# Kernel optimization log

Hardware: AMD Instinct MI355X
Metric: run time of the kernel (lower is better)

Reference implementation:

```python
import jax, jax.numpy as jnp
import numpy as np

B, IN, H, L = 4096, 1024, 1024, 8


def setup_inputs() -> dict:
    key = jax.random.key(0)
    k1, k2, k3, k4, k5 = jax.random.split(key, 5)
    scale = 0.02
    inputs = jax.random.normal(k1, (B, IN), dtype=jnp.float32)
    # Stacked gate weights, order [f, i, o, g] along first axis (torch Linear: y = x @ W.T + b)
    W = jax.random.normal(k2, (4 * H, IN), dtype=jnp.float32) * scale   # input->gates
    bW = jax.random.normal(k3, (4 * H,), dtype=jnp.float32) * scale
    U = jax.random.normal(k4, (4 * H, H), dtype=jnp.float32) * scale    # hidden->gates
    bU = jax.random.normal(k5, (4 * H,), dtype=jnp.float32) * scale
    return {"inputs": inputs, "W": W, "bW": bW, "U": U, "bU": bU, "num_layers": L}


def reference(inputs, W, bW, U, bU, num_layers):
    batch = inputs.shape[0]
    hid = U.shape[1]
    # Input projection is loop-invariant: compute once. [B, 4H]
    x_proj = jnp.einsum('bi,gi->bg', inputs, W) + bW
    xf, xi, xo, xg = jnp.split(x_proj, 4, axis=1)

    def step(carry, _):
        ht, ct = carry
        h_proj = jnp.einsum('bh,gh->bg', ht, U) + bU  # [B, 4H]
        hf, hi, ho, hg = jnp.split(h_proj, 4, axis=1)
        f = jax.nn.sigmoid(xf + hf)
        i = jax.nn.sigmoid(xi + hi)
        o = jax.nn.sigmoid(xo + ho)
        g = jnp.tanh(xg + hg)
        ct_new = f * ct + i * g
        ht_new = o * jnp.tanh(ct_new)
        return (ht_new, ct_new), None

    h0 = jnp.zeros((batch, hid), dtype=inputs.dtype)
    c0 = jnp.zeros((batch, hid), dtype=inputs.dtype)
    (ht, ct), _ = jax.lax.scan(step, (h0, c0), None, length=num_layers)
    return ht, ct
```

## Files before the change

### kernel.cpp

```cpp
#include <hip/hip_runtime.h>
#include <hip/hip_bf16.h>

typedef __bf16 bf16x8 __attribute__((ext_vector_type(8)));
typedef float f32x4 __attribute__((ext_vector_type(4)));

#define DEVI static __device__ __forceinline__

DEVI void load_lds16(const void* g, void* l) {
  __builtin_amdgcn_global_load_lds(
      (const __attribute__((address_space(1))) void*)g,
      (__attribute__((address_space(3))) void*)l, 16, 0, 0);
}

DEVI unsigned short f2b(float f) { return __bfloat16_as_ushort(__float2bfloat16(f)); }
DEVI float b2f(unsigned short u) {
  union { unsigned int i; float f; } c;
  c.i = ((unsigned int)u) << 16;
  return c.f;
}
DEVI float sigm(float x) { return 1.0f / (1.0f + __expf(-x)); }
DEVI float tanh_fast(float x) { return 2.0f / (1.0f + __expf(-2.0f * x)) - 1.0f; }

DEVI int swz(int L) { return L ^ (((L >> 7) & 7) << 4); }

__global__ __launch_bounds__(256) void cast_kernel(const float* __restrict__ src,
                                                   unsigned short* __restrict__ dst,
                                                   int n4) {
  const int i = blockIdx.x * 256 + threadIdx.x;
  if (i >= n4) return;
  const float4 v = reinterpret_cast<const float4*>(src)[i];
  ushort4 o;
  o.x = f2b(v.x); o.y = f2b(v.y); o.z = f2b(v.z); o.w = f2b(v.w);
  reinterpret_cast<ushort4*>(dst)[i] = o;
}

__global__ __launch_bounds__(256) void cast_perm_kernel(const float* __restrict__ src,
                                                        unsigned short* __restrict__ dst) {
  const int i = blockIdx.x * 256 + threadIdx.x;
  const int r = i >> 8;
  const int cw = i & 255;
  const float4 v = reinterpret_cast<const float4*>(src)[i];
  const int rp = ((r & 1023) << 2) + (r >> 10);
  ushort4 o;
  o.x = f2b(v.x); o.y = f2b(v.y); o.z = f2b(v.z); o.w = f2b(v.w);
  *reinterpret_cast<ushort4*>(&dst[(size_t)rp * 1024 + (cw << 2)]) = o;
}

__global__ __launch_bounds__(256) void bias_prep(const float* __restrict__ bW,
                                                 const float* __restrict__ bU,
                                                 float* __restrict__ bp) {
  const int i = blockIdx.x * 256 + threadIdx.x;
  const int h = i >> 2, g = i & 3;
  bp[i] = bW[g * 1024 + h] + bU[g * 1024 + h];
}

template <bool FUSED, bool LAST>
__global__ __launch_bounds__(512, 2) void gemm256(
    const unsigned short* __restrict__ A,
    const unsigned short* __restrict__ Bm,
    unsigned short* __restrict__ Cout,
    const unsigned short* __restrict__ xproj,
    const float* __restrict__ bp,
    float* __restrict__ ct,
    unsigned short* __restrict__ htout,
    float* __restrict__ out) {
  constexpr int K = 1024, N = 4096;
  constexpr int NPH = K / 32;
  __shared__ unsigned char lds[256 * 528];

  const int tid = threadIdx.x;
  const int lane = tid & 63;
  const int wave = tid >> 6;
  const int wr = wave >> 2;
  const int wc = wave & 3;

  const int bid = blockIdx.x;
  const int sw = (bid & 7) * 32 + (bid >> 3);
  const int brow = (sw >> 4) * 256;
  const int bcol = (sw & 15) * 256;

  const int physA0 = tid * 16;
  const int physA1 = 8192 + tid * 16;
  const int physB0 = 16384 + tid * 16;
  const int physB1 = 24576 + tid * 16;
  const int LA0 = swz(physA0), LA1 = swz(physA1);
  const int LB0 = swz(physB0 - 16384), LB1 = swz(physB1 - 16384);
  const unsigned char* pA0 = (const unsigned char*)A + (size_t)(brow + (LA0 >> 6)) * (K * 2) + (LA0 & 63);
  const unsigned char* pA1 = (const unsigned char*)A + (size_t)(brow + (LA1 >> 6)) * (K * 2) + (LA1 & 63);
  const unsigned char* pB0 = (const unsigned char*)Bm + (size_t)(bcol + (LB0 >> 6)) * (K * 2) + (LB0 & 63);
  const unsigned char* pB1 = (const unsigned char*)Bm + (size_t)(bcol + (LB1 >> 6)) * (K * 2) + (LB1 & 63);

  const int s16 = (lane >> 4) * 16;
  int offA[8], offB[4];
#pragma unroll
  for (int m = 0; m < 8; ++m) {
    const int row = wr * 128 + m * 16 + (lane & 15);
    offA[m] = swz(row * 64 + s16);
  }
#pragma unroll
  for (int n = 0; n < 4; ++n) {
    const int row = wc * 64 + n * 16 + (lane & 15);
    offB[n] = 16384 + swz(row * 64 + s16);
  }

  f32x4 acc[8][4] = {};

  auto STAGE = [&](int q) {
    unsigned char* sb = lds + (q & 3) * 32768;
    const size_t kb = (size_t)q * 64;
    load_lds16(pA0 + kb, sb + physA0);
    load_lds16(pA1 + kb, sb + physA1);
    load_lds16(pB0 + kb, sb + physB0);
    load_lds16(pB1 + kb, sb + physB1);
  };

  STAGE(0); STAGE(1); STAGE(2);
  asm volatile("s_waitcnt vmcnt(8)" ::: "memory");
  __builtin_amdgcn_s_barrier();
  __builtin_amdgcn_sched_barrier(0);

  for (int p = 0; p < NPH; ++p) {
    if (p + 3 < NPH) STAGE(p + 3);

    const unsigned char* sl = lds + (p & 3) * 32768;
    bf16x8 af[8], bf[4];
#pragma unroll
    for (int n = 0; n < 4; ++n) bf[n] = *reinterpret_cast<const bf16x8*>(sl + offB[n]);
#pragma unroll
    for (int m = 0; m < 8; ++m) af[m] = *reinterpret_cast<const bf16x8*>(sl + offA[m]);

    __builtin_amdgcn_s_setprio(1);
#pragma unroll
    for (int m = 0; m < 8; ++m)
#pragma unroll
      for (int n = 0; n < 4; ++n)
        acc[m][n] = __builtin_amdgcn_mfma_f32_16x16x32_bf16(af[m], bf[n], acc[m][n], 0, 0, 0);
    __builtin_amdgcn_s_setprio(0);

    if (p < NPH - 1) {
      if (p < NPH - 3)
        asm volatile("s_waitcnt vmcnt(8)" ::: "memory");
      else if (p == NPH - 3)
        asm volatile("s_waitcnt vmcnt(4)" ::: "memory");
      else
        asm volatile("s_waitcnt vmcnt(0)" ::: "memory");
      __builtin_amdgcn_s_barrier();
      __builtin_amdgcn_sched_barrier(0);
    }
  }

  __syncthreads();
  unsigned short* cs = (unsigned short*)lds;
  {
    const int c0 = wc * 64 + (lane & 15);
    const int r00 = wr * 128 + ((lane >> 4) << 2);
#pragma unroll
    for (int m = 0; m < 8; ++m)
#pragma unroll
      for (int n = 0; n < 4; ++n) {
        const int rr = r00 + m * 16;
        const int cc = c0 + n * 16;
#pragma unroll
        for (int r = 0; r < 4; ++r) cs[(rr + r) * 264 + cc] = f2b(acc[m][n][r]);
      }
  }
  __syncthreads();

  if constexpr (!FUSED) {
#pragma unroll
    for (int j = 0; j < 16; ++j) {
      const int g = tid + (j << 9);
      const int row = g >> 5, gc = g & 31;
      const uint4 v = *reinterpret_cast<const uint4*>(&cs[row * 264 + gc * 8]);
      *reinterpret_cast<uint4*>(&Cout[(size_t)(brow + row) * N + bcol + gc * 8]) = v;
    }
  } else {
    const int hbase = bcol >> 2;
    for (int j = 0; j < 32; ++j) {
      const int q = tid + (j << 9);
      const int row = q >> 6;
      const int hh = q & 63;
      const ushort4 pv = *reinterpret_cast<const ushort4*>(&cs[row * 264 + hh * 4]);
      const ushort4 xv = *reinterpret_cast<const ushort4*>(&xproj[(size_t)(brow + row) * N + bcol + hh * 4]);
      const float4 bpv = *reinterpret_cast<const float4*>(&bp[bcol + hh * 4]);
      const int ci = (brow + row) * 1024 + hbase + hh;
      const float c_old = ct[ci];
      const float sf = b2f(pv.x) + b2f(xv.x) + bpv.x;
      const float si = b2f(pv.y) + b2f(xv.y) + bpv.y;
      const float so = b2f(pv.z) + b2f(xv.z) + bpv.z;
      const float sg = b2f(pv.w) + b2f(xv.w) + bpv.w;
      const float f = sigm(sf);
      const float ii = sigm(si);
      const float o = sigm(so);
      const float gg = tanh_fast(sg);
      const float c = fmaf(f, c_old, ii * gg);
      const float h = o * tanh_fast(c);
      ct[ci] = c;
      if constexpr (LAST) {
        out[ci] = h;
        out[4194304 + ci] = c;
      } else {
        htout[ci] = f2b(h);
      }
    }
  }
}

__global__ __launch_bounds__(256) void gates_first(
    const unsigned short* __restrict__ xproj, const float* __restrict__ bp,
    float* __restrict__ ct, unsigned short* __restrict__ ht) {
  const int i = blockIdx.x * 256 + threadIdx.x;
  const int b = i >> 8;
  const int h0 = (i & 255) << 2;
  const size_t xbase = (size_t)b * 4096 + ((size_t)h0 << 2);
  float cn[4], hn[4];
#pragma unroll
  for (int k = 0; k < 4; ++k) {
    const ushort4 pv = *reinterpret_cast<const ushort4*>(&xproj[xbase + k * 4]);
    const float4 bpv = *reinterpret_cast<const float4*>(&bp[(h0 + k) * 4]);
    const float f = sigm(b2f(pv.x) + bpv.x);  (void)f;
    const float ii = sigm(b2f(pv.y) + bpv.y);
    const float o = sigm(b2f(pv.z) + bpv.z);
    const float gg = tanh_fast(b2f(pv.w) + bpv.w);
    const float c = ii * gg;
    cn[k] = c;
    hn[k] = o * tanh_fast(c);
  }
  const int ci = b * 1024 + h0;
  *reinterpret_cast<float4*>(&ct[ci]) = make_float4(cn[0], cn[1], cn[2], cn[3]);
  ushort4 hb;
  hb.x = f2b(hn[0]); hb.y = f2b(hn[1]); hb.z = f2b(hn[2]); hb.w = f2b(hn[3]);
  *reinterpret_cast<ushort4*>(&ht[ci]) = hb;
}

extern "C" void kernel_launch(void* const* d_in, const int* in_sizes, int n_in,
                              void* d_out, int out_size, void* d_ws, size_t ws_size,
                              hipStream_t stream) {
  const float* x = (const float*)d_in[0];
  const float* W = (const float*)d_in[1];
  const float* bW = (const float*)d_in[2];
  const float* U = (const float*)d_in[3];
  const float* bU = (const float*)d_in[4];
  float* out = (float*)d_out;

  char* w = (char*)d_ws;
  const size_t MB = 1ull << 20;
  unsigned short* xb = (unsigned short*)(w + 0 * MB);
  unsigned short* Wbp = (unsigned short*)(w + 8 * MB);
  unsigned short* Ubp = (unsigned short*)(w + 16 * MB);
  unsigned short* xproj = (unsigned short*)(w + 24 * MB);
  float* ct = (float*)(w + 56 * MB);
  unsigned short* htA = (unsigned short*)(w + 72 * MB);
  unsigned short* htB = (unsigned short*)(w + 80 * MB);
  float* bp = (float*)(w + 88 * MB);

  const int n4 = (4096 * 1024) / 4;
  cast_kernel<<<4096, 256, 0, stream>>>(x, xb, n4);
  cast_perm_kernel<<<4096, 256, 0, stream>>>(W, Wbp);
  cast_perm_kernel<<<4096, 256, 0, stream>>>(U, Ubp);
  bias_prep<<<16, 256, 0, stream>>>(bW, bU, bp);

  gemm256<false, false><<<256, 512, 0, stream>>>(xb, Wbp, xproj, nullptr, nullptr, nullptr, nullptr, nullptr);
  gates_first<<<4096, 256, 0, stream>>>(xproj, bp, ct, htA);

  const unsigned short* hin = htA;
  unsigned short* hout = htB;
  for (int t = 1; t <= 6; ++t) {
    gemm256<true, false><<<256, 512, 0, stream>>>(hin, Ubp, nullptr, xproj, bp, ct, hout, nullptr);
    const unsigned short* tmp = hout;
    hout = (unsigned short*)hin;
    hin = tmp;
  }
  gemm256<true, true><<<256, 512, 0, stream>>>(hin, Ubp, nullptr, xproj, bp, ct, nullptr, out);
}
```

Measured before the change: 428.8 us.

## Shrink GEMM tile to 128x256 with 4 waves and triple buffering

Changes the GEMM block tile from 256x256 with 8 waves to 128x256 with 4 waves, launching 512 blocks instead of 256. The LDS pipeline drops from 4 slots with prefetch depth 3 to 3 slots with depth 2, cutting LDS per block so more blocks can be resident per CU. The aim is better occupancy and load balance across the 256 CUs, at the cost of reloading the B (weight) tile twice as often per output and a shallower prefetch that may expose memory latency. It also drops an unused sigmoid in gates_first and partially unrolls the fused epilogue loop.

After: 443.1 us. 3.3% more time.

```diff
diff --git a/kernel.cpp b/kernel.cpp
--- a/kernel.cpp
+++ b/kernel.cpp
@@ -55,7 +55,7 @@
 }
 
 template <bool FUSED, bool LAST>
-__global__ __launch_bounds__(512, 2) void gemm256(
+__global__ __launch_bounds__(256, 2) void gemm256(
     const unsigned short* __restrict__ A,
     const unsigned short* __restrict__ Bm,
     unsigned short* __restrict__ Cout,
@@ -66,63 +66,59 @@
     float* __restrict__ out) {
   constexpr int K = 1024, N = 4096;
   constexpr int NPH = K / 32;
-  __shared__ unsigned char lds[256 * 528];
+  constexpr int SLOT = 24576;
+  __shared__ unsigned char lds[3 * SLOT];
 
   const int tid = threadIdx.x;
   const int lane = tid & 63;
-  const int wave = tid >> 6;
-  const int wr = wave >> 2;
-  const int wc = wave & 3;
+  const int wc = tid >> 6;
 
   const int bid = blockIdx.x;
-  const int sw = (bid & 7) * 32 + (bid >> 3);
-  const int brow = (sw >> 4) * 256;
+  const int sw = (bid & 7) * 64 + (bid >> 3);
+  const int brow = (sw >> 4) * 128;
   const int bcol = (sw & 15) * 256;
 
   const int physA0 = tid * 16;
-  const int physA1 = 8192 + tid * 16;
-  const int physB0 = 16384 + tid * 16;
-  const int physB1 = 24576 + tid * 16;
+  const int physA1 = 4096 + tid * 16;
   const int LA0 = swz(physA0), LA1 = swz(physA1);
-  const int LB0 = swz(physB0 - 16384), LB1 = swz(physB1 - 16384);
   const unsigned char* pA0 = (const unsigned char*)A + (size_t)(brow + (LA0 >> 6)) * (K * 2) + (LA0 & 63);
   const unsigned char* pA1 = (const unsigned char*)A + (size_t)(brow + (LA1 >> 6)) * (K * 2) + (LA1 & 63);
-  const unsigned char* pB0 = (const unsigned char*)Bm + (size_t)(bcol + (LB0 >> 6)) * (K * 2) + (LB0 & 63);
-  const unsigned char* pB1 = (const unsigned char*)Bm + (size_t)(bcol + (LB1 >> 6)) * (K * 2) + (LB1 & 63);
+  int physB[4];
+  const unsigned char* pB[4];
+#pragma unroll
+  for (int q = 0; q < 4; ++q) {
+    physB[q] = 8192 + q * 4096 + tid * 16;
+    const int LB = swz(physB[q] - 8192);
+    pB[q] = (const unsigned char*)Bm + (size_t)(bcol + (LB >> 6)) * (K * 2) + (LB & 63);
+  }
 
   const int s16 = (lane >> 4) * 16;
   int offA[8], offB[4];
 #pragma unroll
-  for (int m = 0; m < 8; ++m) {
-    const int row = wr * 128 + m * 16 + (lane & 15);
-    offA[m] = swz(row * 64 + s16);
-  }
-#pragma unroll
-  for (int n = 0; n < 4; ++n) {
-    const int row = wc * 64 + n * 16 + (lane & 15);
-    offB[n] = 16384 + swz(row * 64 + s16);
-  }
+  for (int m = 0; m < 8; ++m) offA[m] = swz((m * 16 + (lane & 15)) * 64 + s16);
+#pragma unroll
+  for (int n = 0; n < 4; ++n) offB[n] = 8192 + swz(((wc * 64) + n * 16 + (lane & 15)) * 64 + s16);
 
   f32x4 acc[8][4] = {};
 
   auto STAGE = [&](int q) {
-    unsigned char* sb = lds + (q & 3) * 32768;
+    unsigned char* sb = lds + (q % 3) * SLOT;
     const size_t kb = (size_t)q * 64;
     load_lds16(pA0 + kb, sb + physA0);
     load_lds16(pA1 + kb, sb + physA1);
-    load_lds16(pB0 + kb, sb + physB0);
-    load_lds16(pB1 + kb, sb + physB1);
+#pragma unroll
+    for (int j = 0; j < 4; ++j) load_lds16(pB[j] + kb, sb + physB[j]);
   };
 
-  STAGE(0); STAGE(1); STAGE(2);
-  asm volatile("s_waitcnt vmcnt(8)" ::: "memory");
+  STAGE(0); STAGE(1);
+  asm volatile("s_waitcnt vmcnt(6)" ::: "memory");
   __builtin_amdgcn_s_barrier();
   __builtin_amdgcn_sched_barrier(0);
 
   for (int p = 0; p < NPH; ++p) {
-    if (p + 3 < NPH) STAGE(p + 3);
-
-    const unsigned char* sl = lds + (p & 3) * 32768;
+    if (p + 2 < NPH) STAGE(p + 2);
+
+    const unsigned char* sl = lds + (p % 3) * SLOT;
     bf16x8 af[8], bf[4];
 #pragma unroll
     for (int n = 0; n < 4; ++n) bf[n] = *reinterpret_cast<const bf16x8*>(sl + offB[n]);
@@ -138,10 +134,8 @@
     __builtin_amdgcn_s_setprio(0);
 
     if (p < NPH - 1) {
-      if (p < NPH - 3)
-        asm volatile("s_waitcnt vmcnt(8)" ::: "memory");
-      else if (p == NPH - 3)
-        asm volatile("s_waitcnt vmcnt(4)" ::: "memory");
+      if (p <= NPH - 3)
+        asm volatile("s_waitcnt vmcnt(6)" ::: "memory");
       else
         asm volatile("s_waitcnt vmcnt(0)" ::: "memory");
       __builtin_amdgcn_s_barrier();
@@ -153,12 +147,12 @@
   unsigned short* cs = (unsigned short*)lds;
   {
     const int c0 = wc * 64 + (lane & 15);
-    const int r00 = wr * 128 + ((lane >> 4) << 2);
+    const int crow0 = (lane >> 4) * 4;
 #pragma unroll
     for (int m = 0; m < 8; ++m)
 #pragma unroll
       for (int n = 0; n < 4; ++n) {
-        const int rr = r00 + m * 16;
+        const int rr = m * 16 + crow0;
         const int cc = c0 + n * 16;
 #pragma unroll
         for (int r = 0; r < 4; ++r) cs[(rr + r) * 264 + cc] = f2b(acc[m][n][r]);
@@ -169,15 +163,16 @@
   if constexpr (!FUSED) {
 #pragma unroll
     for (int j = 0; j < 16; ++j) {
-      const int g = tid + (j << 9);
+      const int g = tid + (j << 8);
       const int row = g >> 5, gc = g & 31;
       const uint4 v = *reinterpret_cast<const uint4*>(&cs[row * 264 + gc * 8]);
       *reinterpret_cast<uint4*>(&Cout[(size_t)(brow + row) * N + bcol + gc * 8]) = v;
     }
   } else {
     const int hbase = bcol >> 2;
+#pragma unroll 4
     for (int j = 0; j < 32; ++j) {
-      const int q = tid + (j << 9);
+      const int q = tid + (j << 8);
       const int row = q >> 6;
       const int hh = q & 63;
       const ushort4 pv = *reinterpret_cast<const ushort4*>(&cs[row * 264 + hh * 4]);
@@ -218,7 +213,6 @@
   for (int k = 0; k < 4; ++k) {
     const ushort4 pv = *reinterpret_cast<const ushort4*>(&xproj[xbase + k * 4]);
     const float4 bpv = *reinterpret_cast<const float4*>(&bp[(h0 + k) * 4]);
-    const float f = sigm(b2f(pv.x) + bpv.x);  (void)f;
     const float ii = sigm(b2f(pv.y) + bpv.y);
     const float o = sigm(b2f(pv.z) + bpv.z);
     const float gg = tanh_fast(b2f(pv.w) + bpv.w);
@@ -260,16 +254,16 @@
   cast_perm_kernel<<<4096, 256, 0, stream>>>(U, Ubp);
   bias_prep<<<16, 256, 0, stream>>>(bW, bU, bp);
 
-  gemm256<false, false><<<256, 512, 0, stream>>>(xb, Wbp, xproj, nullptr, nullptr, nullptr, nullptr, nullptr);
+  gemm256<false, false><<<512, 256, 0, stream>>>(xb, Wbp, xproj, nullptr, nullptr, nullptr, nullptr, nullptr);
   gates_first<<<4096, 256, 0, stream>>>(xproj, bp, ct, htA);
 
   const unsigned short* hin = htA;
   unsigned short* hout = htB;
   for (int t = 1; t <= 6; ++t) {
-    gemm256<true, false><<<256, 512, 0, stream>>>(hin, Ubp, nullptr, xproj, bp, ct, hout, nullptr);
+    gemm256<true, false><<<512, 256, 0, stream>>>(hin, Ubp, nullptr, xproj, bp, ct, hout, nullptr);
     const unsigned short* tmp = hout;
     hout = (unsigned short*)hin;
     hin = tmp;
   }
-  gemm256<true, true><<<256, 512, 0, stream>>>(hin, Ubp, nullptr, xproj, bp, ct, nullptr, out);
-}
+  gemm256<true, true><<<512, 256, 0, stream>>>(hin, Ubp, nullptr, xproj, bp, ct, nullptr, out);
+}
```

## Fuse first-step gates into input GEMM, fold bias into xproj, store cell state in bf16

Applied to the files above, without the earlier changes.

The input-projection GEMM now also computes the first LSTM step's gates and writes h and c directly, which removes the separate gates_first kernel and one full re-read of xproj. The combined bias is added once and stored into the bf16 xproj buffer, so later steps no longer load the bias. The cell state is kept in bf16 instead of fp32, which halves its read/write traffic per step. Storing c in bf16 across steps loses precision and can accumulate error over the recurrence.

Result: faster. 402.6 us (-6.1%).

```diff
diff --git a/kernel.cpp b/kernel.cpp
--- a/kernel.cpp
+++ b/kernel.cpp
@@ -54,14 +54,14 @@
   bp[i] = bW[g * 1024 + h] + bU[g * 1024 + h];
 }
 
-template <bool FUSED, bool LAST>
+template <int MODE>
 __global__ __launch_bounds__(512, 2) void gemm256(
     const unsigned short* __restrict__ A,
     const unsigned short* __restrict__ Bm,
-    unsigned short* __restrict__ Cout,
-    const unsigned short* __restrict__ xproj,
+    const unsigned short* __restrict__ xpb_r,
+    unsigned short* __restrict__ xpb_w,
     const float* __restrict__ bp,
-    float* __restrict__ ct,
+    unsigned short* __restrict__ ct,
     unsigned short* __restrict__ htout,
     float* __restrict__ out) {
   constexpr int K = 1024, N = 4096;
@@ -166,71 +166,46 @@
   }
   __syncthreads();
 
-  if constexpr (!FUSED) {
-#pragma unroll
-    for (int j = 0; j < 16; ++j) {
-      const int g = tid + (j << 9);
-      const int row = g >> 5, gc = g & 31;
-      const uint4 v = *reinterpret_cast<const uint4*>(&cs[row * 264 + gc * 8]);
-      *reinterpret_cast<uint4*>(&Cout[(size_t)(brow + row) * N + bcol + gc * 8]) = v;
+  const int hbase = bcol >> 2;
+#pragma unroll 4
+  for (int j = 0; j < 32; ++j) {
+    const int q = tid + (j << 9);
+    const int row = q >> 6;
+    const int hh = q & 63;
+    const ushort4 pv = *reinterpret_cast<const ushort4*>(&cs[row * 264 + hh * 4]);
+    const int ci = (brow + row) * 1024 + hbase + hh;
+    float sf, si, so, sg;
+    if constexpr (MODE == 0) {
+      const float4 bpv = *reinterpret_cast<const float4*>(&bp[bcol + hh * 4]);
+      sf = b2f(pv.x) + bpv.x;
+      si = b2f(pv.y) + bpv.y;
+      so = b2f(pv.z) + bpv.z;
+      sg = b2f(pv.w) + bpv.w;
+      ushort4 xo;
+      xo.x = f2b(sf); xo.y = f2b(si); xo.z = f2b(so); xo.w = f2b(sg);
+      *reinterpret_cast<ushort4*>(&xpb_w[(size_t)(brow + row) * N + bcol + hh * 4]) = xo;
+    } else {
+      const ushort4 xv = *reinterpret_cast<const ushort4*>(&xpb_r[(size_t)(brow + row) * N + bcol + hh * 4]);
+      sf = b2f(pv.x) + b2f(xv.x);
+      si = b2f(pv.y) + b2f(xv.y);
+      so = b2f(pv.z) + b2f(xv.z);
+      sg = b2f(pv.w) + b2f(xv.w);
     }
-  } else {
-    const int hbase = bcol >> 2;
-    for (int j = 0; j < 32; ++j) {
-      const int q = tid + (j << 9);
-      const int row = q >> 6;
-      const int hh = q & 63;
-      const ushort4 pv = *reinterpret_cast<const ushort4*>(&cs[row * 264 + hh * 4]);
-      const ushort4 xv = *reinterpret_cast<const ushort4*>(&xproj[(size_t)(brow + row) * N + bcol + hh * 4]);
-      const float4 bpv = *reinterpret_cast<const float4*>(&bp[bcol + hh * 4]);
-      const int ci = (brow + row) * 1024 + hbase + hh;
-      const float c_old = ct[ci];
-      const float sf = b2f(pv.x) + b2f(xv.x) + bpv.x;
-      const float si = b2f(pv.y) + b2f(xv.y) + bpv.y;
-      const float so = b2f(pv.z) + b2f(xv.z) + bpv.z;
-      const float sg = b2f(pv.w) + b2f(xv.w) + bpv.w;
-      const float f = sigm(sf);
-      const float ii = sigm(si);
-      const float o = sigm(so);
-      const float gg = tanh_fast(sg);
-      const float c = fmaf(f, c_old, ii * gg);
-      const float h = o * tanh_fast(c);
-      ct[ci] = c;
-      if constexpr (LAST) {
-        out[ci] = h;
-        out[4194304 + ci] = c;
-      } else {
-        htout[ci] = f2b(h);
-      }
+    const float c_old = (MODE == 0) ? 0.0f : b2f(ct[ci]);
+    const float f = sigm(sf);
+    const float ii = sigm(si);
+    const float o = sigm(so);
+    const float gg = tanh_fast(sg);
+    const float c = fmaf(f, c_old, ii * gg);
+    const float h = o * tanh_fast(c);
+    if constexpr (MODE == 2) {
+      out[ci] = h;
+      out[4194304 + ci] = c;
+    } else {
+      ct[ci] = f2b(c);
+      htout[ci] = f2b(h);
     }
   }
-}
-
-__global__ __launch_bounds__(256) void gates_first(
-    const unsigned short* __restrict__ xproj, const float* __restrict__ bp,
-    float* __restrict__ ct, unsigned short* __restrict__ ht) {
-  const int i = blockIdx.x * 256 + threadIdx.x;
-  const int b = i >> 8;
-  const int h0 = (i & 255) << 2;
-  const size_t xbase = (size_t)b * 4096 + ((size_t)h0 << 2);
-  float cn[4], hn[4];
-#pragma unroll
-  for (int k = 0; k < 4; ++k) {
-    const ushort4 pv = *reinterpret_cast<const ushort4*>(&xproj[xbase + k * 4]);
-    const float4 bpv = *reinterpret_cast<const float4*>(&bp[(h0 + k) * 4]);
-    const float f = sigm(b2f(pv.x) + bpv.x);  (void)f;
-    const float ii = sigm(b2f(pv.y) + bpv.y);
-    const float o = sigm(b2f(pv.z) + bpv.z);
-    const float gg = tanh_fast(b2f(pv.w) + bpv.w);
-    const float c = ii * gg;
-    cn[k] = c;
-    hn[k] = o * tanh_fast(c);
-  }
-  const int ci = b * 1024 + h0;
-  *reinterpret_cast<float4*>(&ct[ci]) = make_float4(cn[0], cn[1], cn[2], cn[3]);
-  ushort4 hb;
-  hb.x = f2b(hn[0]); hb.y = f2b(hn[1]); hb.z = f2b(hn[2]); hb.w = f2b(hn[3]);
-  *reinterpret_cast<ushort4*>(&ht[ci]) = hb;
 }
 
 extern "C" void kernel_launch(void* const* d_in, const int* in_sizes, int n_in,
@@ -248,11 +223,11 @@
   unsigned short* xb = (unsigned short*)(w + 0 * MB);
   unsigned short* Wbp = (unsigned short*)(w + 8 * MB);
   unsigned short* Ubp = (unsigned short*)(w + 16 * MB);
-  unsigned short* xproj = (unsigned short*)(w + 24 * MB);
-  float* ct = (float*)(w + 56 * MB);
-  unsigned short* htA = (unsigned short*)(w + 72 * MB);
-  unsigned short* htB = (unsigned short*)(w + 80 * MB);
-  float* bp = (float*)(w + 88 * MB);
+  unsigned short* xpb = (unsigned short*)(w + 24 * MB);
+  unsigned short* ct = (unsigned short*)(w + 56 * MB);
+  unsigned short* htA = (unsigned short*)(w + 64 * MB);
+  unsigned short* htB = (unsigned short*)(w + 72 * MB);
+  float* bp = (float*)(w + 80 * MB);
 
   const int n4 = (4096 * 1024) / 4;
   cast_kernel<<<4096, 256, 0, stream>>>(x, xb, n4);
@@ -260,16 +235,15 @@
   cast_perm_kernel<<<4096, 256, 0, stream>>>(U, Ubp);
   bias_prep<<<16, 256, 0, stream>>>(bW, bU, bp);
 
-  gemm256<false, false><<<256, 512, 0, stream>>>(xb, Wbp, xproj, nullptr, nullptr, nullptr, nullptr, nullptr);
-  gates_first<<<4096, 256, 0, stream>>>(xproj, bp, ct, htA);
+  gemm256<0><<<256, 512, 0, stream>>>(xb, Wbp, nullptr, xpb, bp, ct, htA, nullptr);
 
   const unsigned short* hin = htA;
   unsigned short* hout = htB;
   for (int t = 1; t <= 6; ++t) {
-    gemm256<true, false><<<256, 512, 0, stream>>>(hin, Ubp, nullptr, xproj, bp, ct, hout, nullptr);
+    gemm256<1><<<256, 512, 0, stream>>>(hin, Ubp, xpb, nullptr, nullptr, ct, hout, nullptr);
     const unsigned short* tmp = hout;
     hout = (unsigned short*)hin;
     hin = tmp;
   }
-  gemm256<true, true><<<256, 512, 0, stream>>>(hin, Ubp, nullptr, xproj, bp, ct, nullptr, out);
-}
+  gemm256<2><<<256, 512, 0, stream>>>(hin, Ubp, xpb, nullptr, nullptr, ct, nullptr, out);
+}
```
